# Kernel optimization log

Measured on AMD Instinct MI355X. Metric: run time of the kernel, lower is better.

The kernel has to match this reference:

```python
import jax, jax.numpy as jnp
import numpy as np

NUM_PTS = 1024
LATENT_SIZE = 32
BETA = 0.1


def setup_inputs() -> dict:
    key = jax.random.key(0)
    k1, k2, k3, k4 = jax.random.split(key, 4)
    B = 128
    return {
        "recon_x": jax.random.normal(k1, (B, NUM_PTS, 3), dtype=jnp.float32),
        "x": jax.random.normal(k2, (B, NUM_PTS, 3), dtype=jnp.float32),
        "mu": jax.random.normal(k3, (B, LATENT_SIZE), dtype=jnp.float32),
        "logvar": jax.random.normal(k4, (B, LATENT_SIZE), dtype=jnp.float32),
    }


def _chamfer(recon_x, x):
    # Batched squared pairwise distances: P[b, i, j] = ||x[b,i] - recon_x[b,j]||^2
    xx = jnp.sum(x * x, axis=-1)              # [B, N]
    yy = jnp.sum(recon_x * recon_x, axis=-1)  # [B, N]
    xy = jnp.einsum("bnd,bmd->bnm", x, recon_x)  # [B, N, N]
    P = xx[:, :, None] + yy[:, None, :] - 2.0 * xy
    # Bidirectional min + sum
    loss_1 = jnp.sum(jnp.min(P, axis=1))  # for each recon point, nearest x point
    loss_2 = jnp.sum(jnp.min(P, axis=2))  # for each x point, nearest recon point
    return loss_1 + loss_2


def reference(recon_x, x, mu, logvar):
    RE = _chamfer(recon_x, x) / NUM_PTS
    KLD = -0.5 * jnp.sum(1.0 + logvar - mu * mu - jnp.exp(logvar))
    KLD = KLD / LATENT_SIZE
    return RE + KLD * BETA
```

## Files before the change

### kernel.cpp

```cpp
#include <hip/hip_runtime.h>

#define NUM_PTS 1024
#define NBATCH 128
#define BT 512
#define NW 8
#define QW 128
#define R 8
#define NSTEP 64
#define CHAMF_SCALE (1.0f / 1024.0f)
#define KLD_SCALE   (-0.5f * 0.1f / 32.0f)

#define COL_OFF 0
#define RS_OFF  (256 * 1024)
#define WS2_OFF (RS_OFF + 256)

__global__ __launch_bounds__(BT, 4) void chamfer_shared(
    const float* __restrict__ recon_x,
    const float* __restrict__ x,
    float* __restrict__ ws)
{
    const int bid = blockIdx.x;
    const int b   = bid >> 1;
    const int rh  = bid & 1;
    const int w   = threadIdx.x >> 6;
    const int lt  = threadIdx.x & 63;
    const int t   = threadIdx.x;

    __shared__ float4 ring[NW][2][2 * NSTEP];
    __shared__ float  comb[NW][BT];
    __shared__ float  red[NW];

    {
        const float* qsrc = recon_x + (size_t)b * NUM_PTS * 3 + (size_t)(w * QW) * 3;
#pragma unroll
        for (int i = 0; i < 2; ++i) {
            const int c = i * 64 + lt;
            const float qx = qsrc[3 * c + 0];
            const float qy = qsrc[3 * c + 1];
            const float qz = qsrc[3 * c + 2];
            const float4 q4 = make_float4(qx, qy, qz,
                                          fmaf(qx, qx, fmaf(qy, qy, qz * qz)));
            ring[w][i][lt]      = q4;
            ring[w][i][lt + 64] = q4;
        }
    }

    const float* rp = x + (size_t)b * NUM_PTS * 3 + (size_t)rh * 512 * 3;
    float vx[R], vy[R], vz[R], r2[R], m[R];
    {
        float buf[24];
        const float4* __restrict__ s4 = (const float4*)(rp + 24 * lt);
        float4* bp = (float4*)buf;
#pragma unroll
        for (int i = 0; i < 6; ++i) bp[i] = s4[i];
#pragma unroll
        for (int k = 0; k < R; ++k) {
            vx[k] = -2.0f * buf[3 * k + 0];
            vy[k] = -2.0f * buf[3 * k + 1];
            vz[k] = -2.0f * buf[3 * k + 2];
            r2[k] = 0.25f * fmaf(vx[k], vx[k], fmaf(vy[k], vy[k], vz[k] * vz[k]));
            m[k]  = 1e30f;
        }
    }

    const float4* __restrict__ r0 = &ring[w][0][lt];
    const float4* __restrict__ r1 = &ring[w][1][lt];
    float ca = 1e30f, cb = 1e30f;
    const int rotaddr = ((lt + 1) & 63) << 2;

#pragma unroll 16
    for (int s = 0; s < NSTEP; ++s) {
        const float4 qa = r0[s];
        const float4 qb = r1[s];
        float da[R], db[R];
#pragma unroll
        for (int r = 0; r < R; ++r) {
            da[r] = fmaf(vx[r], qa.x, fmaf(vy[r], qa.y, fmaf(vz[r], qa.z, r2[r] + qa.w)));
            db[r] = fmaf(vx[r], qb.x, fmaf(vy[r], qb.y, fmaf(vz[r], qb.z, r2[r] + qb.w)));
        }
#pragma unroll
        for (int r = 0; r < R; ++r)
            m[r] = fminf(fminf(m[r], da[r]), db[r]);
        {
            const float t0 = fminf(fminf(da[0], da[1]), da[2]);
            const float t1 = fminf(fminf(da[3], da[4]), da[5]);
            const float t2 = fminf(fminf(da[6], da[7]), ca);
            ca = fminf(fminf(t0, t1), t2);
        }
        {
            const float u0 = fminf(fminf(db[0], db[1]), db[2]);
            const float u1 = fminf(fminf(db[3], db[4]), db[5]);
            const float u2 = fminf(fminf(db[6], db[7]), cb);
            cb = fminf(fminf(u0, u1), u2);
        }
        ca = __int_as_float(__builtin_amdgcn_ds_bpermute(rotaddr, __float_as_int(ca)));
        cb = __int_as_float(__builtin_amdgcn_ds_bpermute(rotaddr, __float_as_int(cb)));
    }

    {
        float* cp = ws + COL_OFF + (size_t)bid * 1024 + w * QW;
        cp[lt]      = ca;
        cp[64 + lt] = cb;
    }

#pragma unroll
    for (int k = 0; k < R; ++k)
        comb[w][R * lt + k] = m[k];
    __syncthreads();

    float v = comb[0][t];
#pragma unroll
    for (int ww = 1; ww < NW; ++ww) v = fminf(v, comb[ww][t]);
    for (int off = 32; off > 0; off >>= 1)
        v += __shfl_down(v, off, 64);
    if (lt == 0) red[w] = v;
    __syncthreads();
    if (t == 0) {
        float s = 0.f;
#pragma unroll
        for (int ww = 0; ww < NW; ++ww) s += red[ww];
        ws[RS_OFF + bid] = s;
    }
}

__global__ __launch_bounds__(256) void colfold(float* __restrict__ ws)
{
    const int b = blockIdx.x;
    const int t = threadIdx.x;
    const float4* p0 = (const float4*)(ws + COL_OFF + (size_t)(2 * b)     * 1024) + t;
    const float4* p1 = (const float4*)(ws + COL_OFF + (size_t)(2 * b + 1) * 1024) + t;
    const float4 a = *p0;
    const float4 c = *p1;
    float v = fminf(a.x, c.x) + fminf(a.y, c.y) + fminf(a.z, c.z) + fminf(a.w, c.w);
    for (int off = 32; off > 0; off >>= 1)
        v += __shfl_down(v, off, 64);
    __shared__ float red[4];
    if ((t & 63) == 0) red[t >> 6] = v;
    __syncthreads();
    if (t == 0) {
        float s = red[0] + red[1] + red[2] + red[3];
        s += ws[RS_OFF + 2 * b] + ws[RS_OFF + 2 * b + 1];
        ws[WS2_OFF + b] = s;
    }
}

__global__ __launch_bounds__(128) void final_k(
    const float* __restrict__ ws,
    const float* __restrict__ mu,
    const float* __restrict__ logvar,
    float* __restrict__ out)
{
    const int t = threadIdx.x;
    float v = ws[WS2_OFF + t] * CHAMF_SCALE;

    const float4* mp = (const float4*)mu + 8 * t;
    const float4* lp = (const float4*)logvar + 8 * t;
    float kv = 0.f;
#pragma unroll
    for (int i = 0; i < 8; ++i) {
        const float4 mm = mp[i];
        const float4 lv = lp[i];
        kv += (1.f + lv.x - mm.x * mm.x - expf(lv.x));
        kv += (1.f + lv.y - mm.y * mm.y - expf(lv.y));
        kv += (1.f + lv.z - mm.z * mm.z - expf(lv.z));
        kv += (1.f + lv.w - mm.w * mm.w - expf(lv.w));
    }
    v += kv * KLD_SCALE;

    for (int off = 32; off > 0; off >>= 1)
        v += __shfl_down(v, off, 64);
    __shared__ float red[2];
    if ((t & 63) == 0) red[t >> 6] = v;
    __syncthreads();
    if (t == 0) out[0] = red[0] + red[1];
}

extern "C" void kernel_launch(void* const* d_in, const int* in_sizes, int n_in,
                              void* d_out, int out_size, void* d_ws, size_t ws_size,
                              hipStream_t stream) {
    const float* recon_x = (const float*)d_in[0];
    const float* x       = (const float*)d_in[1];
    const float* mu      = (const float*)d_in[2];
    const float* logvar  = (const float*)d_in[3];
    float* out = (float*)d_out;
    float* ws  = (float*)d_ws;

    chamfer_shared<<<2 * NBATCH, BT, 0, stream>>>(recon_x, x, ws);
    colfold<<<NBATCH, 256, 0, stream>>>(ws);
    final_k<<<1, 128, 0, stream>>>(ws, mu, logvar, out);
}
```

Baseline: 78.73 us.

## Double waves per block, halve query columns per wave, reuse ring for reduction

Doubles the block to 1024 threads (16 waves). Each wave now owns 64 query columns instead of 128, and a single rotating column-min register replaces the two separate chains, with a bpermute after each half-step. The shared ring is padded and reused as the row-min scratch, which drops the separate comb array, and q values are prefetched one iteration ahead. The goal is more resident waves per CU to hide latency, but launch_bounds(1024,4) may force a tight VGPR cap and cause spills, and the per-wave column rotation chain is now serialized.

```diff
diff --git a/kernel.cpp b/kernel.cpp
--- a/kernel.cpp
+++ b/kernel.cpp
@@ -2,11 +2,12 @@
 
 #define NUM_PTS 1024
 #define NBATCH 128
-#define BT 512
-#define NW 8
-#define QW 128
+#define BT 1024
+#define NW 16
+#define QW 64
 #define R 8
 #define NSTEP 64
+#define RING_PAD 132
 #define CHAMF_SCALE (1.0f / 1024.0f)
 #define KLD_SCALE   (-0.5f * 0.1f / 32.0f)
 
@@ -26,23 +27,16 @@
     const int lt  = threadIdx.x & 63;
     const int t   = threadIdx.x;
 
-    __shared__ float4 ring[NW][2][2 * NSTEP];
-    __shared__ float  comb[NW][BT];
+    __shared__ float4 ring[NW][RING_PAD];
     __shared__ float  red[NW];
 
     {
-        const float* qsrc = recon_x + (size_t)b * NUM_PTS * 3 + (size_t)(w * QW) * 3;
-#pragma unroll
-        for (int i = 0; i < 2; ++i) {
-            const int c = i * 64 + lt;
-            const float qx = qsrc[3 * c + 0];
-            const float qy = qsrc[3 * c + 1];
-            const float qz = qsrc[3 * c + 2];
-            const float4 q4 = make_float4(qx, qy, qz,
-                                          fmaf(qx, qx, fmaf(qy, qy, qz * qz)));
-            ring[w][i][lt]      = q4;
-            ring[w][i][lt + 64] = q4;
-        }
+        const float* qsrc = recon_x + (size_t)b * NUM_PTS * 3 + (size_t)(w * QW + lt) * 3;
+        const float qx = qsrc[0], qy = qsrc[1], qz = qsrc[2];
+        const float4 q4 = make_float4(qx, qy, qz,
+                                      fmaf(qx, qx, fmaf(qy, qy, qz * qz)));
+        ring[w][lt]      = q4;
+        ring[w][lt + 64] = q4;
     }
 
     const float* rp = x + (size_t)b * NUM_PTS * 3 + (size_t)rh * 512 * 3;
@@ -63,62 +57,70 @@
         }
     }
 
-    const float4* __restrict__ r0 = &ring[w][0][lt];
-    const float4* __restrict__ r1 = &ring[w][1][lt];
-    float ca = 1e30f, cb = 1e30f;
+    const float4* __restrict__ ringw = &ring[w][lt];
+    float ca = 1e30f;
     const int rotaddr = ((lt + 1) & 63) << 2;
+    float4 qA = ringw[0];
+    float4 qB = ringw[1];
 
-#pragma unroll 16
-    for (int s = 0; s < NSTEP; ++s) {
-        const float4 qa = r0[s];
-        const float4 qb = r1[s];
+#pragma unroll 4
+    for (int s = 0; s < NSTEP; s += 2) {
+        const float4 qC = ringw[s + 2];
+        const float4 qD = ringw[s + 3];
         float da[R], db[R];
 #pragma unroll
-        for (int r = 0; r < R; ++r) {
-            da[r] = fmaf(vx[r], qa.x, fmaf(vy[r], qa.y, fmaf(vz[r], qa.z, r2[r] + qa.w)));
-            db[r] = fmaf(vx[r], qb.x, fmaf(vy[r], qb.y, fmaf(vz[r], qb.z, r2[r] + qb.w)));
-        }
-#pragma unroll
         for (int r = 0; r < R; ++r)
-            m[r] = fminf(fminf(m[r], da[r]), db[r]);
+            da[r] = fmaf(vx[r], qA.x, fmaf(vy[r], qA.y, fmaf(vz[r], qA.z, r2[r] + qA.w)));
         {
             const float t0 = fminf(fminf(da[0], da[1]), da[2]);
             const float t1 = fminf(fminf(da[3], da[4]), da[5]);
             const float t2 = fminf(fminf(da[6], da[7]), ca);
             ca = fminf(fminf(t0, t1), t2);
         }
+        ca = __int_as_float(__builtin_amdgcn_ds_bpermute(rotaddr, __float_as_int(ca)));
+#pragma unroll
+        for (int r = 0; r < R; ++r)
+            db[r] = fmaf(vx[r], qB.x, fmaf(vy[r], qB.y, fmaf(vz[r], qB.z, r2[r] + qB.w)));
+#pragma unroll
+        for (int r = 0; r < R; ++r)
+            m[r] = fminf(fminf(m[r], da[r]), db[r]);
         {
             const float u0 = fminf(fminf(db[0], db[1]), db[2]);
             const float u1 = fminf(fminf(db[3], db[4]), db[5]);
-            const float u2 = fminf(fminf(db[6], db[7]), cb);
-            cb = fminf(fminf(u0, u1), u2);
+            const float u2 = fminf(fminf(db[6], db[7]), ca);
+            ca = fminf(fminf(u0, u1), u2);
         }
         ca = __int_as_float(__builtin_amdgcn_ds_bpermute(rotaddr, __float_as_int(ca)));
-        cb = __int_as_float(__builtin_amdgcn_ds_bpermute(rotaddr, __float_as_int(cb)));
+        qA = qC;
+        qB = qD;
     }
 
+    ws[COL_OFF + (size_t)bid * 1024 + w * QW + lt] = ca;
+
     {
-        float* cp = ws + COL_OFF + (size_t)bid * 1024 + w * QW;
-        cp[lt]      = ca;
-        cp[64 + lt] = cb;
+        float* mrow = (float*)&ring[w][0];
+#pragma unroll
+        for (int k = 0; k < R; ++k)
+            mrow[R * lt + k] = m[k];
     }
-
-#pragma unroll
-    for (int k = 0; k < R; ++k)
-        comb[w][R * lt + k] = m[k];
     __syncthreads();
 
-    float v = comb[0][t];
+    float v = 0.0f;
+    if (t < 512) {
+        const float* cb = (const float*)&ring[0][0];
+        v = cb[t];
 #pragma unroll
-    for (int ww = 1; ww < NW; ++ww) v = fminf(v, comb[ww][t]);
-    for (int off = 32; off > 0; off >>= 1)
-        v += __shfl_down(v, off, 64);
-    if (lt == 0) red[w] = v;
+        for (int ww = 1; ww < NW; ++ww)
+            v = fminf(v, cb[ww * (RING_PAD * 4) + t]);
+        for (int off = 32; off > 0; off >>= 1)
+            v += __shfl_down(v, off, 64);
+        if (lt == 0) red[w] = v;
+    }
     __syncthreads();
     if (t == 0) {
         float s = 0.f;
 #pragma unroll
-        for (int ww = 0; ww < NW; ++ww) s += red[ww];
+        for (int ww = 0; ww < 8; ++ww) s += red[ww];
         ws[RS_OFF + bid] = s;
     }
 }
```

Result: no change. 77.80 us (-1.2%).
